# Kernel optimization log

Hardware: AMD Instinct MI355X
Metric: run time of the kernel (lower is better)

Reference implementation:

```python
import jax, jax.numpy as jnp
import numpy as np

TOKENS, D_IN = 8192, 1024
E, D_OUT = 8, 1024
H = 2 * D_OUT  # Expert hidden = 2 * num_outputs


def setup_inputs() -> dict:
    key = jax.random.key(0)
    ks = jax.random.split(key, 4)
    s_in = 1.0 / np.sqrt(D_IN)
    s_h = 1.0 / np.sqrt(H)
    return {
        "x": jax.random.normal(ks[0], (TOKENS, D_IN), dtype=jnp.float32),
        "W1": jax.random.normal(ks[1], (E, D_IN, H), dtype=jnp.float32) * s_in,
        "b1": jnp.zeros((E, H), dtype=jnp.float32),
        "W2": jax.random.normal(ks[2], (E, H, D_OUT), dtype=jnp.float32) * s_h,
        "b2": jnp.zeros((E, D_OUT), dtype=jnp.float32),
        "Wg": jax.random.normal(ks[3], (D_IN, E), dtype=jnp.float32) * s_in,
        "bg": jnp.zeros((E,), dtype=jnp.float32),
    }


def reference(x, W1, b1, W2, b2, Wg, bg):
    # Gating: softmax over experts. gates: [N, E]
    gates = jax.nn.softmax(x @ Wg + bg, axis=-1)
    # All experts run densely: batched GEMM over expert axis.
    h = jax.nn.relu(jnp.einsum('nd,edh->neh', x, W1) + b1)       # [N, E, H]
    expert_out = jnp.einsum('neh,ehf->nef', h, W2) + b2          # [N, E, D_OUT]
    # Gate-weighted sum over experts (fused stack*gate->sum).
    return jnp.einsum('nef,ne->nf', expert_out, gates)            # [N, D_OUT]
```

## Files before the change

### kernel.cpp

```cpp
#include <hip/hip_runtime.h>
#include <stdint.h>

#define TOKENS 8192
#define D_IN   1024
#define NEXP   8
#define D_OUT  1024
#define HDIM   2048

typedef __bf16 bf16x8 __attribute__((ext_vector_type(8)));
typedef __bf16 bf16x4 __attribute__((ext_vector_type(4)));
typedef float  f32x4  __attribute__((ext_vector_type(4)));

__device__ __forceinline__ void gload16(const void* g, void* l) {
  __builtin_amdgcn_global_load_lds(
      (const __attribute__((address_space(1))) void*)g,
      (__attribute__((address_space(3))) void*)l,
      16, 0, 0);
}

template <int N>
__device__ __forceinline__ void waitv() {
  if constexpr (N == 0)      asm volatile("s_waitcnt vmcnt(0)" ::: "memory");
  else if constexpr (N == 1) asm volatile("s_waitcnt vmcnt(1)" ::: "memory");
  else if constexpr (N == 2) asm volatile("s_waitcnt vmcnt(2)" ::: "memory");
  else if constexpr (N == 3) asm volatile("s_waitcnt vmcnt(3)" ::: "memory");
  else if constexpr (N == 4) asm volatile("s_waitcnt vmcnt(4)" ::: "memory");
  else if constexpr (N == 5) asm volatile("s_waitcnt vmcnt(5)" ::: "memory");
  else if constexpr (N == 6) asm volatile("s_waitcnt vmcnt(6)" ::: "memory");
  else static_assert(N <= 6, "unsupported vmcnt");
}

__global__ void gate_cvt_kernel(const float* __restrict__ x,
                                const float* __restrict__ Wg,
                                const float* __restrict__ bg,
                                float* __restrict__ gates,
                                __bf16* __restrict__ xb) {
  const int lane = threadIdx.x & 63;
  const int n = blockIdx.x * 4 + (threadIdx.x >> 6);
  float acc[NEXP];
#pragma unroll
  for (int e = 0; e < NEXP; ++e) acc[e] = 0.f;
  const float* xr = x + (size_t)n * D_IN;
  __bf16* xo = xb + (size_t)n * D_IN;
#pragma unroll 4
  for (int d0 = 0; d0 < D_IN; d0 += 64) {
    const int d = d0 + lane;
    float xv = xr[d];
    xo[d] = (__bf16)xv;
    const float* wr = Wg + d * NEXP;
#pragma unroll
    for (int e = 0; e < NEXP; ++e) acc[e] += xv * wr[e];
  }
#pragma unroll
  for (int e = 0; e < NEXP; ++e) {
    float v = acc[e];
#pragma unroll
    for (int off = 32; off > 0; off >>= 1) v += __shfl_down(v, off);
    acc[e] = v;
  }
  if (lane == 0) {
    float mx = -1e30f;
#pragma unroll
    for (int e = 0; e < NEXP; ++e) { acc[e] += bg[e]; mx = fmaxf(mx, acc[e]); }
    float s = 0.f;
#pragma unroll
    for (int e = 0; e < NEXP; ++e) { acc[e] = expf(acc[e] - mx); s += acc[e]; }
    float inv = 1.f / s;
#pragma unroll
    for (int e = 0; e < NEXP; ++e) gates[n * NEXP + e] = acc[e] * inv;
  }
}

__global__ void transpose_cvt_kernel(const float* __restrict__ W,
                                     __bf16* __restrict__ Wt,
                                     int K, int N, int EPG) {
  __shared__ float tile[32][33];
  const int e = blockIdx.z;
  const int ldo = EPG * K;
  const float* Win = W + (size_t)e * K * N;
  __bf16* Wout = Wt + (size_t)(e / EPG) * N * ldo + (size_t)(e % EPG) * K;
  const int n0 = blockIdx.x * 32;
  const int k0 = blockIdx.y * 32;
  const int tx = threadIdx.x & 31;
  const int ty = threadIdx.x >> 5;
#pragma unroll
  for (int r = ty; r < 32; r += 8)
    tile[r][tx] = Win[(size_t)(k0 + r) * N + n0 + tx];
  __syncthreads();
#pragma unroll
  for (int r = ty; r < 32; r += 8)
    Wout[(size_t)(n0 + r) * ldo + k0 + tx] = (__bf16)tile[tx][r];
}

__global__ void merge_kernel(float* __restrict__ out,
                             const float* __restrict__ acc1,
                             const float* __restrict__ gates,
                             const float* __restrict__ b2,
                             int use_acc1) {
  const int idx = blockIdx.x * 256 + threadIdx.x;
  const int n = idx >> 8;
  const int fb = idx & 255;
  float4 o = ((const float4*)out)[idx];
  if (use_acc1) {
    float4 a = ((const float4*)acc1)[idx];
    o.x += a.x; o.y += a.y; o.z += a.z; o.w += a.w;
  }
  const float* g = gates + (size_t)n * NEXP;
#pragma unroll
  for (int e = 0; e < NEXP; ++e) {
    const float ge = g[e];
    float4 b = ((const float4*)(b2 + (size_t)e * D_OUT))[fb];
    o.x += ge * b.x; o.y += ge * b.y; o.z += ge * b.z; o.w += ge * b.w;
  }
  ((float4*)out)[idx] = o;
}

template <int NT, int BM, int BN, int WM, int WN, int EPI, int DBUF>
__global__ __launch_bounds__(NT, 2)
void moe_gemm(const __bf16* __restrict__ A, size_t AZ,
              const __bf16* __restrict__ B, size_t BZ,
              const float* __restrict__ b1g,
              const float* __restrict__ gates,
              int e0,
              __bf16* __restrict__ Hout, size_t HZ, int OCZ, int ldo,
              float* __restrict__ F0, float* __restrict__ F1,
              int first, int M, int N, int K) {
  constexpr int RM = BM / WM, RN = BN / WN;
  constexpr int FM = RM / 16, FN = RN / 16;
  constexpr int HM = FM / 2,  HN = FN / 2;
  constexpr int LA = BM * 4 / NT;
  constexpr int LB = BN * 4 / NT;
  constexpr int AELEM = BM * 64;
  constexpr int SLOT  = (BM + BN) * 64;
  static_assert(HM * HN * 2 == 16, "want 16-MFMA quadrant clusters");
  __shared__ alignas(16) __bf16 lds[DBUF * SLOT];

  const int tid  = threadIdx.x;
  const int lane = tid & 63;
  const int wave = tid >> 6;
  const int wr   = wave / WN;
  const int wc   = wave % WN;
  const int lrow = lane & 15;
  const int khi  = lane >> 4;
  const int sx   = (lrow & 7) << 3;
  const int bz   = blockIdx.z;

  A += (size_t)bz * AZ;
  B += (size_t)bz * BZ;

  const int Gx   = gridDim.x;
  const int nwg  = Gx * gridDim.y;
  const int orig = blockIdx.y * Gx + blockIdx.x;
  const int wgid = (orig & 7) * (nwg >> 3) + (orig >> 3);
  const int bn0  = (wgid % Gx) * BN;
  const int bm0  = (wgid / Gx) * BM;

  const __bf16* srcA[2][LA];
  const __bf16* srcB[2][LB];
#pragma unroll
  for (int q = 0; q < 2; ++q) {
#pragma unroll
    for (int j = 0; j < LA; ++j) {
      int o   = q * (BM * 64) + j * (NT * 16) + tid * 16;
      int row = o >> 7;
      int cb  = (o & 127) ^ ((row & 7) << 4);
      srcA[q][j] = A + (size_t)(bm0 + row) * K + (cb >> 1);
    }
#pragma unroll
    for (int j = 0; j < LB; ++j) {
      int o   = q * (BN * 64) + j * (NT * 16) + tid * 16;
      int row = o >> 7;
      int cb  = (o & 127) ^ ((row & 7) << 4);
      srcB[q][j] = B + (size_t)(bn0 + row) * K + (cb >> 1);
    }
  }

  auto stageA = [&](int kt, int q, int s) {
#pragma unroll
    for (int j = 0; j < LA; ++j)
      gload16(srcA[q][j] + (size_t)kt * 64,
              lds + s * SLOT + q * (BM * 32) + j * (NT * 8) + wave * 512);
  };
  auto stageB = [&](int kt, int q, int s) {
#pragma unroll
    for (int j = 0; j < LB; ++j)
      gload16(srcB[q][j] + (size_t)kt * 64,
              lds + s * SLOT + AELEM + q * (BN * 32) + j * (NT * 8) + wave * 512);
  };

  f32x4 acc[FM][FN];
#pragma unroll
  for (int m = 0; m < FM; ++m)
#pragma unroll
    for (int n = 0; n < FN; ++n) acc[m][n] = f32x4{0.f, 0.f, 0.f, 0.f};

  bf16x8 af[HM][2];
  bf16x8 bf[2][HN][2];

  auto rdA = [&](const __bf16* As, int mq) {
#pragma unroll
    for (int mi = 0; mi < HM; ++mi)
#pragma unroll
      for (int kk = 0; kk < 2; ++kk)
        af[mi][kk] = *(const bf16x8*)
            &As[(size_t)(mq * (BM / 2) + wr * (RM / 2) + mi * 16 + lrow) * 64 +
                ((kk * 32 + khi * 8) ^ sx)];
  };
  auto rdB = [&](const __bf16* Bs, int nq) {
#pragma unroll
    for (int ni = 0; ni < HN; ++ni)
#pragma unroll
      for (int kk = 0; kk < 2; ++kk)
        bf[nq][ni][kk] = *(const bf16x8*)
            &Bs[(size_t)(nq * (BN / 2) + wc * (RN / 2) + ni * 16 + lrow) * 64 +
                ((kk * 32 + khi * 8) ^ sx)];
  };
  auto cluster = [&](int mq, int nq) {
    __builtin_amdgcn_s_setprio(1);
#pragma unroll
    for (int kk = 0; kk < 2; ++kk)
#pragma unroll
      for (int mi = 0; mi < HM; ++mi)
#pragma unroll
        for (int ni = 0; ni < HN; ++ni)
          acc[mq * HM + mi][nq * HN + ni] =
              __builtin_amdgcn_mfma_f32_16x16x32_bf16(
                  af[mi][kk], bf[nq][ni][kk], acc[mq * HM + mi][nq * HN + ni],
                  0, 0, 0);
    __builtin_amdgcn_s_setprio(0);
  };
  auto cluster_h = [&](int mq) {
    __builtin_amdgcn_s_setprio(1);
#pragma unroll
    for (int kk = 0; kk < 2; ++kk)
#pragma unroll
      for (int mi = 0; mi < HM; ++mi)
#pragma unroll
        for (int nq = 0; nq < 2; ++nq)
#pragma unroll
          for (int ni = 0; ni < HN; ++ni)
            acc[mq * HM + mi][nq * HN + ni] =
                __builtin_amdgcn_mfma_f32_16x16x32_bf16(
                    af[mi][kk], bf[nq][ni][kk], acc[mq * HM + mi][nq * HN + ni],
                    0, 0, 0);
    __builtin_amdgcn_s_setprio(0);
  };

#define BAR()   asm volatile("s_barrier" ::: "memory")
#define LGKM0() do { asm volatile("s_waitcnt lgkmcnt(0)" ::: "memory"); \
                     __builtin_amdgcn_sched_barrier(0); } while (0)

  const int nk = K >> 6;

  if constexpr (DBUF == 1) {
    stageA(0, 0, 0); stageB(0, 0, 0); stageB(0, 1, 0);
    waitv<LB>();
    BAR();
    for (int t = 0; t < nk; ++t) {
      const bool pf = (t + 1 < nk);
      rdA(lds, 0); rdB(lds + AELEM, 0);
      stageA(t, 1, 0);
      BAR(); LGKM0();
      cluster(0, 0);
      waitv<LA>();
      BAR();
      rdB(lds + AELEM, 1);
      if (pf) stageA(t + 1, 0, 0);
      BAR(); LGKM0();
      cluster(0, 1);
      if (pf) waitv<LA>(); else waitv<0>();
      BAR();
      rdA(lds, 1);
      if (pf) stageB(t + 1, 0, 0);
      BAR(); LGKM0();
      cluster(1, 0);
      BAR();
      if (pf) stageB(t + 1, 1, 0);
      BAR();
      cluster(1, 1);
      if (pf) waitv<LB>();
      BAR();
    }
  } else {
    stageA(0, 0, 0); stageB(0, 0, 0); stageB(0, 1, 0); stageA(0, 1, 0);
    waitv<LA>();
    BAR();
    for (int t = 0; t < nk; ++t) {
      const int s = t & 1;
      const __bf16* As = lds + s * SLOT;
      const __bf16* Bs = As + AELEM;
      const bool pf = (t + 1 < nk);
      rdA(As, 0); rdB(Bs, 0); rdB(Bs, 1);
      if (pf) { stageA(t + 1, 0, s ^ 1); stageB(t + 1, 0, s ^ 1); }
      BAR(); LGKM0();
      cluster_h(0);
      if (pf) waitv<LA + LB>(); else waitv<0>();
      BAR();
      rdA(As, 1);
      if (pf) { stageB(t + 1, 1, s ^ 1); stageA(t + 1, 1, s ^ 1); }
      BAR(); LGKM0();
      cluster_h(1);
      if (pf) waitv<LA>();
      BAR();
    }
  }

#undef BAR
#undef LGKM0

  const float* bias = (EPI == 0) ? b1g + (size_t)(e0 + bz) * HDIM : nullptr;
  const int ecol = e0 + bz;
  __bf16* Hp = (EPI == 0) ? Hout + (size_t)bz * HZ + (size_t)bz * OCZ : nullptr;
  float* F = (EPI == 3) ? (bz ? F1 : F0) : nullptr;

#pragma unroll
  for (int m = 0; m < FM; ++m) {
    const int grow0 = bm0 + (m / HM) * (BM / 2) + wr * (RM / 2) +
                      (m % HM) * 16 + khi * 4;
    if constexpr (EPI == 0) {
      float g[4];
#pragma unroll
      for (int r = 0; r < 4; ++r)
        g[r] = gates[(size_t)(grow0 + r) * NEXP + ecol];
#pragma unroll
      for (int n = 0; n < FN; ++n) {
        const int gcol = bn0 + (n / HN) * (BN / 2) + wc * (RN / 2) +
                         (n % HN) * 16 + lrow;
        const float bv = bias[gcol];
        f32x4 a = acc[m][n];
#pragma unroll
        for (int r = 0; r < 4; ++r) {
          float v = a[r] + bv;
          v = v > 0.f ? v : 0.f;
          Hp[(size_t)(grow0 + r) * ldo + gcol] = (__bf16)(v * g[r]);
        }
      }
    } else {
#pragma unroll
      for (int n = 0; n < FN; ++n) {
        const int gcol = bn0 + (n / HN) * (BN / 2) + wc * (RN / 2) +
                         (n % HN) * 16 + lrow;
        f32x4 a = acc[m][n];
#pragma unroll
        for (int r = 0; r < 4; ++r) {
          float* o = F + (size_t)(grow0 + r) * N + gcol;
          if (first) *o = a[r];
          else       *o += a[r];
        }
      }
    }
  }
}

extern "C" void kernel_launch(void* const* d_in, const int* in_sizes, int n_in,
                              void* d_out, int out_size, void* d_ws, size_t ws_size,
                              hipStream_t stream) {
  const float* x  = (const float*)d_in[0];
  const float* W1 = (const float*)d_in[1];
  const float* b1 = (const float*)d_in[2];
  const float* W2 = (const float*)d_in[3];
  const float* b2 = (const float*)d_in[4];
  const float* Wg = (const float*)d_in[5];
  const float* bg = (const float*)d_in[6];
  float* out = (float*)d_out;

  char* w = (char*)d_ws;
  float* gates = (float*)w;   w += (size_t)TOKENS * NEXP * 4;
  __bf16* xb   = (__bf16*)w;  w += (size_t)TOKENS * D_IN * 2;
  __bf16* w1t  = (__bf16*)w;  w += (size_t)NEXP * HDIM * D_IN * 2;
  __bf16* w2c  = (__bf16*)w;  w += (size_t)NEXP * D_OUT * HDIM * 2;
  const size_t base = (size_t)(w - (char*)d_ws);

  const size_t acc_b = (size_t)TOKENS * D_OUT * 4;
  const size_t h1_b  = (size_t)TOKENS * HDIM * 2;
  const int G = (ws_size >= base + acc_b + 4 * h1_b) ? 4
              : (ws_size >= base + acc_b + 2 * h1_b) ? 2 : 1;

  float* acc1 = nullptr;
  if (G > 1) { acc1 = (float*)w; w += acc_b; }
  __bf16* hbuf = (__bf16*)w;

  const size_t WSLICE = (size_t)HDIM * D_IN;

  gate_cvt_kernel<<<TOKENS / 4, 256, 0, stream>>>(x, Wg, bg, gates, xb);
  transpose_cvt_kernel<<<dim3(HDIM / 32, D_IN / 32, NEXP), 256, 0, stream>>>(
      W1, w1t, D_IN, HDIM, 1);
  transpose_cvt_kernel<<<dim3(D_OUT / 32, HDIM / 32, NEXP), 256, 0, stream>>>(
      W2, w2c, HDIM, D_OUT, (G == 4) ? 2 : 1);

  if (G == 4) {
    for (int d = 0; d < 2; ++d) {
      for (int i2 = 0; i2 < 2; ++i2) {
        const int e0 = 4 * d + 2 * i2;
        moe_gemm<512, 256, 256, 2, 4, 0, 1><<<dim3(8, 32, 2), 512, 0, stream>>>(
            xb, 0, w1t + (size_t)e0 * WSLICE, WSLICE, b1, gates, e0,
            hbuf + (size_t)i2 * TOKENS * 4096, 0, HDIM, 2 * HDIM,
            nullptr, nullptr, 0, TOKENS, HDIM, D_IN);
      }
      moe_gemm<512, 256, 256, 2, 4, 3, 2><<<dim3(4, 32, 2), 512, 0, stream>>>(
          hbuf, (size_t)TOKENS * 4096,
          w2c + (size_t)(2 * d) * D_OUT * 4096, (size_t)D_OUT * 4096,
          nullptr, nullptr, 0, nullptr, 0, 0, 0,
          out, acc1, (d == 0) ? 1 : 0, TOKENS, D_OUT, 2 * HDIM);
    }
  } else if (G == 2) {
    for (int d = 0; d < 4; ++d) {
      const int e0 = 2 * d;
      moe_gemm<512, 256, 256, 2, 4, 0, 1><<<dim3(8, 32, 2), 512, 0, stream>>>(
          xb, 0, w1t + (size_t)e0 * WSLICE, WSLICE, b1, gates, e0,
          hbuf, (size_t)TOKENS * HDIM, 0, HDIM,
          nullptr, nullptr, 0, TOKENS, HDIM, D_IN);
      moe_gemm<512, 256, 256, 2, 4, 3, 2><<<dim3(4, 32, 2), 512, 0, stream>>>(
          hbuf, (size_t)TOKENS * HDIM,
          w2c + (size_t)e0 * D_OUT * HDIM, (size_t)D_OUT * HDIM,
          nullptr, nullptr, 0, nullptr, 0, 0, 0,
          out, acc1, (d == 0) ? 1 : 0, TOKENS, D_OUT, HDIM);
    }
  } else {
    for (int e = 0; e < NEXP; ++e) {
      moe_gemm<512, 256, 256, 2, 4, 0, 1><<<dim3(8, 32, 1), 512, 0, stream>>>(
          xb, 0, w1t + (size_t)e * WSLICE, 0, b1, gates, e,
          hbuf, 0, 0, HDIM,
          nullptr, nullptr, 0, TOKENS, HDIM, D_IN);
      moe_gemm<512, 256, 256, 2, 4, 3, 2><<<dim3(4, 32, 1), 512, 0, stream>>>(
          hbuf, 0, w2c + (size_t)e * D_OUT * HDIM, 0,
          nullptr, nullptr, 0, nullptr, 0, 0, 0,
          out, nullptr, (e == 0) ? 1 : 0, TOKENS, D_OUT, HDIM);
    }
  }

  merge_kernel<<<TOKENS, 256, 0, stream>>>(out, acc1, gates, b2, (G > 1) ? 1 : 0);
}
```

Baseline: 669.5 us.

## Stage second-GEMM tiles through registers with two-deep prefetch instead of direct-to-LDS loads

```diff
diff --git a/kernel.cpp b/kernel.cpp
--- a/kernel.cpp
+++ b/kernel.cpp
@@ -25,9 +25,9 @@
   else if constexpr (N == 2) asm volatile("s_waitcnt vmcnt(2)" ::: "memory");
   else if constexpr (N == 3) asm volatile("s_waitcnt vmcnt(3)" ::: "memory");
   else if constexpr (N == 4) asm volatile("s_waitcnt vmcnt(4)" ::: "memory");
-  else if constexpr (N == 5) asm volatile("s_waitcnt vmcnt(5)" ::: "memory");
   else if constexpr (N == 6) asm volatile("s_waitcnt vmcnt(6)" ::: "memory");
-  else static_assert(N <= 6, "unsupported vmcnt");
+  else if constexpr (N == 8) asm volatile("s_waitcnt vmcnt(8)" ::: "memory");
+  else static_assert(N <= 8, "unsupported vmcnt");
 }
 
 __global__ void gate_cvt_kernel(const float* __restrict__ x,
@@ -130,10 +130,12 @@
   constexpr int HM = FM / 2,  HN = FN / 2;
   constexpr int LA = BM * 4 / NT;
   constexpr int LB = BN * 4 / NT;
+  constexpr int TILE = 2 * LA + 2 * LB;
   constexpr int AELEM = BM * 64;
   constexpr int SLOT  = (BM + BN) * 64;
+  constexpr int NSLOT = (DBUF == 1) ? 1 : 2;
   static_assert(HM * HN * 2 == 16, "want 16-MFMA quadrant clusters");
-  __shared__ alignas(16) __bf16 lds[DBUF * SLOT];
+  __shared__ alignas(16) __bf16 lds[NSLOT * SLOT];
 
   const int tid  = threadIdx.x;
   const int lane = tid & 63;
@@ -155,39 +157,6 @@
   const int bn0  = (wgid % Gx) * BN;
   const int bm0  = (wgid / Gx) * BM;
 
-  const __bf16* srcA[2][LA];
-  const __bf16* srcB[2][LB];
-#pragma unroll
-  for (int q = 0; q < 2; ++q) {
-#pragma unroll
-    for (int j = 0; j < LA; ++j) {
-      int o   = q * (BM * 64) + j * (NT * 16) + tid * 16;
-      int row = o >> 7;
-      int cb  = (o & 127) ^ ((row & 7) << 4);
-      srcA[q][j] = A + (size_t)(bm0 + row) * K + (cb >> 1);
-    }
-#pragma unroll
-    for (int j = 0; j < LB; ++j) {
-      int o   = q * (BN * 64) + j * (NT * 16) + tid * 16;
-      int row = o >> 7;
-      int cb  = (o & 127) ^ ((row & 7) << 4);
-      srcB[q][j] = B + (size_t)(bn0 + row) * K + (cb >> 1);
-    }
-  }
-
-  auto stageA = [&](int kt, int q, int s) {
-#pragma unroll
-    for (int j = 0; j < LA; ++j)
-      gload16(srcA[q][j] + (size_t)kt * 64,
-              lds + s * SLOT + q * (BM * 32) + j * (NT * 8) + wave * 512);
-  };
-  auto stageB = [&](int kt, int q, int s) {
-#pragma unroll
-    for (int j = 0; j < LB; ++j)
-      gload16(srcB[q][j] + (size_t)kt * 64,
-              lds + s * SLOT + AELEM + q * (BN * 32) + j * (NT * 8) + wave * 512);
-  };
-
   f32x4 acc[FM][FN];
 #pragma unroll
   for (int m = 0; m < FM; ++m)
@@ -253,55 +222,138 @@
   const int nk = K >> 6;
 
   if constexpr (DBUF == 1) {
-    stageA(0, 0, 0); stageB(0, 0, 0); stageB(0, 1, 0);
+    const __bf16* srcA[2][LA];
+    const __bf16* srcB[2][LB];
+#pragma unroll
+    for (int q = 0; q < 2; ++q) {
+#pragma unroll
+      for (int j = 0; j < LA; ++j) {
+        int o   = q * (BM * 64) + j * (NT * 16) + tid * 16;
+        int row = o >> 7;
+        int cb  = (o & 127) ^ ((row & 7) << 4);
+        srcA[q][j] = A + (size_t)(bm0 + row) * K + (cb >> 1);
+      }
+#pragma unroll
+      for (int j = 0; j < LB; ++j) {
+        int o   = q * (BN * 64) + j * (NT * 16) + tid * 16;
+        int row = o >> 7;
+        int cb  = (o & 127) ^ ((row & 7) << 4);
+        srcB[q][j] = B + (size_t)(bn0 + row) * K + (cb >> 1);
+      }
+    }
+    auto stageA = [&](int kt, int q) {
+#pragma unroll
+      for (int j = 0; j < LA; ++j)
+        gload16(srcA[q][j] + (size_t)kt * 64,
+                lds + q * (BM * 32) + j * (NT * 8) + wave * 512);
+    };
+    auto stageB = [&](int kt, int q) {
+#pragma unroll
+      for (int j = 0; j < LB; ++j)
+        gload16(srcB[q][j] + (size_t)kt * 64,
+                lds + AELEM + q * (BN * 32) + j * (NT * 8) + wave * 512);
+    };
+
+    stageA(0, 0); stageB(0, 0); stageB(0, 1);
     waitv<LB>();
     BAR();
     for (int t = 0; t < nk; ++t) {
       const bool pf = (t + 1 < nk);
       rdA(lds, 0); rdB(lds + AELEM, 0);
-      stageA(t, 1, 0);
+      stageA(t, 1);
       BAR(); LGKM0();
       cluster(0, 0);
       waitv<LA>();
       BAR();
       rdB(lds + AELEM, 1);
-      if (pf) stageA(t + 1, 0, 0);
+      if (pf) stageA(t + 1, 0);
       BAR(); LGKM0();
       cluster(0, 1);
       if (pf) waitv<LA>(); else waitv<0>();
       BAR();
       rdA(lds, 1);
-      if (pf) stageB(t + 1, 0, 0);
+      if (pf) stageB(t + 1, 0);
       BAR(); LGKM0();
       cluster(1, 0);
       BAR();
-      if (pf) stageB(t + 1, 1, 0);
+      if (pf) stageB(t + 1, 1);
       BAR();
       cluster(1, 1);
       if (pf) waitv<LB>();
       BAR();
     }
   } else {
-    stageA(0, 0, 0); stageB(0, 0, 0); stageB(0, 1, 0); stageA(0, 1, 0);
-    waitv<LA>();
+    static_assert(TILE == 8, "reg-staged path sized for 256x256 tiles");
+    const __bf16* srcLin[8];
+    int dstSwz[8];
+#pragma unroll
+    for (int i = 0; i < 8; ++i) {
+      int o    = i * (NT * 16) + tid * 16;
+      bool isA = (o < BM * 128);
+      int oo   = isA ? o : (o - BM * 128);
+      int row  = oo >> 7;
+      int colb = oo & 127;
+      srcLin[i] = (isA ? A + (size_t)(bm0 + row) * K
+                       : B + (size_t)(bn0 + row) * K) + (colb >> 1);
+      dstSwz[i] = (isA ? 0 : BM * 128) +
+                  ((oo & ~127) | (colb ^ ((row & 7) << 4)));
+    }
+    auto issue = [&](int kt, float4* R) {
+#pragma unroll
+      for (int i = 0; i < 8; ++i)
+        R[i] = *reinterpret_cast<const float4*>(srcLin[i] + (size_t)kt * 64);
+    };
+    auto wstage = [&](const float4* R, int s) {
+      char* base = (char*)lds + (size_t)s * (SLOT * 2);
+#pragma unroll
+      for (int i = 0; i < 8; ++i)
+        *reinterpret_cast<float4*>(base + dstSwz[i]) = R[i];
+    };
+
+    float4 R0[8], R1[8];
+    issue(0, R0); issue(1, R1);
+    waitv<8>();
+    wstage(R0, 0);
+    LGKM0();
     BAR();
-    for (int t = 0; t < nk; ++t) {
-      const int s = t & 1;
-      const __bf16* As = lds + s * SLOT;
-      const __bf16* Bs = As + AELEM;
-      const bool pf = (t + 1 < nk);
-      rdA(As, 0); rdB(Bs, 0); rdB(Bs, 1);
-      if (pf) { stageA(t + 1, 0, s ^ 1); stageB(t + 1, 0, s ^ 1); }
-      BAR(); LGKM0();
-      cluster_h(0);
-      if (pf) waitv<LA + LB>(); else waitv<0>();
-      BAR();
-      rdA(As, 1);
-      if (pf) { stageB(t + 1, 1, s ^ 1); stageA(t + 1, 1, s ^ 1); }
-      BAR(); LGKM0();
-      cluster_h(1);
-      if (pf) waitv<LA>();
-      BAR();
+
+    const int half = nk >> 1;
+    for (int tt = 0; tt < half; ++tt) {
+      {
+        const int t = 2 * tt;
+        const __bf16* As = lds;
+        const __bf16* Bs = lds + AELEM;
+        const bool pf2 = (t + 2 < nk);
+        rdA(As, 0); rdB(Bs, 0); rdB(Bs, 1);
+        if (pf2) issue(t + 2, R0);
+        LGKM0();
+        cluster_h(0);
+        rdA(As, 1);
+        if (pf2) waitv<8>(); else waitv<0>();
+        wstage(R1, 1);
+        LGKM0();
+        cluster_h(1);
+        BAR();
+      }
+      {
+        const int t = 2 * tt + 1;
+        const __bf16* As = lds + SLOT;
+        const __bf16* Bs = As + AELEM;
+        const bool pf1 = (t + 1 < nk);
+        const bool pf2 = (t + 2 < nk);
+        rdA(As, 0); rdB(Bs, 0); rdB(Bs, 1);
+        if (pf2) issue(t + 2, R1);
+        LGKM0();
+        cluster_h(0);
+        rdA(As, 1);
+        if (pf1) {
+          if (pf2) waitv<8>(); else waitv<0>();
+          wstage(R0, 0);
+        }
+        LGKM0();
+        cluster_h(1);
+        BAR();
+      }
     }
   }
 
@@ -397,7 +449,7 @@
             hbuf + (size_t)i2 * TOKENS * 4096, 0, HDIM, 2 * HDIM,
             nullptr, nullptr, 0, TOKENS, HDIM, D_IN);
       }
-      moe_gemm<512, 256, 256, 2, 4, 3, 2><<<dim3(4, 32, 2), 512, 0, stream>>>(
+      moe_gemm<512, 256, 256, 2, 4, 3, 3><<<dim3(4, 32, 2), 512, 0, stream>>>(
           hbuf, (size_t)TOKENS * 4096,
           w2c + (size_t)(2 * d) * D_OUT * 4096, (size_t)D_OUT * 4096,
           nullptr, nullptr, 0, nullptr, 0, 0, 0,
@@ -410,7 +462,7 @@
           xb, 0, w1t + (size_t)e0 * WSLICE, WSLICE, b1, gates, e0,
           hbuf, (size_t)TOKENS * HDIM, 0, HDIM,
           nullptr, nullptr, 0, TOKENS, HDIM, D_IN);
-      moe_gemm<512, 256, 256, 2, 4, 3, 2><<<dim3(4, 32, 2), 512, 0, stream>>>(
+      moe_gemm<512, 256, 256, 2, 4, 3, 3><<<dim3(4, 32, 2), 512, 0, stream>>>(
           hbuf, (size_t)TOKENS * HDIM,
           w2c + (size_t)e0 * D_OUT * HDIM, (size_t)D_OUT * HDIM,
           nullptr, nullptr, 0, nullptr, 0, 0, 0,
@@ -422,7 +474,7 @@
           xb, 0, w1t + (size_t)e * WSLICE, 0, b1, gates, e,
           hbuf, 0, 0, HDIM,
           nullptr, nullptr, 0, TOKENS, HDIM, D_IN);
-      moe_gemm<512, 256, 256, 2, 4, 3, 2><<<dim3(4, 32, 1), 512, 0, stream>>>(
+      moe_gemm<512, 256, 256, 2, 4, 3, 3><<<dim3(4, 32, 1), 512, 0, stream>>>(
           hbuf, 0, w2c + (size_t)e * D_OUT * HDIM, 0,
           nullptr, nullptr, 0, nullptr, 0, 0, 0,
           out, nullptr, (e == 0) ? 1 : 0, TOKENS, D_OUT, HDIM);
```

Result: slower. 1.778 ms (+165.6%).
